# Performance work log

Hardware: AMD Instinct MI355X
Metric: run time of the kernel (lower is better)

Reference implementation:

```python
import jax, jax.numpy as jnp
import numpy as np

N_OBJECTS = 64
EMB = 64
N_PRED = 32
N_LAYERS = 3
BATCH = 128

# Ordered pairs (i, j), i != j, in the exact nested-loop order of the torch module
_pairs = np.array([(i, j) for i in range(N_OBJECTS) for j in range(N_OBJECTS) if i != j], dtype=np.int32)
IDX_I = jnp.asarray(_pairs[:, 0])  # [N*(N-1)]
IDX_J = jnp.asarray(_pairs[:, 1])


def setup_inputs() -> dict:
    key = jax.random.key(0)
    ks = jax.random.split(key, 5)
    return {
        "object_ids": jax.random.randint(ks[0], (BATCH, N_OBJECTS), 0, N_OBJECTS),
        "emb_table": jax.random.normal(ks[1], (N_OBJECTS, EMB), dtype=jnp.float32),
        "W1": jax.random.normal(ks[2], (N_LAYERS, EMB, 3 * EMB), dtype=jnp.float32) * 0.07,
        "b1": jnp.zeros((N_LAYERS, EMB), dtype=jnp.float32),
        "W2": jax.random.normal(ks[3], (N_LAYERS, N_PRED, EMB), dtype=jnp.float32) * 0.12,
        "b2": jnp.zeros((N_LAYERS, N_PRED), dtype=jnp.float32),
    }


def reference(object_ids, emb_table, W1, b1, W2, b2):
    e = emb_table[object_ids]                # [B, N, D] embedding lookup
    mean = e.mean(axis=1)                    # [B, D] — identical for every pair (torch recomputes it)
    B, _, D = e.shape
    P = IDX_I.shape[0]                       # N*(N-1) ordered pairs
    # triple = cat([e_i, e_j, mean]) for all ordered pairs, built once: [B, P, 3D]
    triple = jnp.concatenate(
        [e[:, IDX_I, :], e[:, IDX_J, :], jnp.broadcast_to(mean[:, None, :], (B, P, D))],
        axis=-1,
    )
    # All layers share the same triple input; batch all pairs into single GEMMs per layer.
    h = jax.nn.relu(jnp.einsum('bpc,ldc->lbpd', triple, W1) + b1[:, None, None, :])   # [L,B,P,D]
    preds = jax.nn.sigmoid(jnp.einsum('lbpd,lqd->lbpq', h, W2) + b2[:, None, None, :])  # [L,B,P,Q]
    return preds, e
```

## Files before the change

kernel.cpp:

```cpp
#include <hip/hip_runtime.h>
#include <hip/hip_bf16.h>
#include <math.h>

#define NL 3
#define NB 128
#define NO 64
#define ND 64
#define NQ 32
#define NP 4032

typedef __bf16 bf16x8 __attribute__((ext_vector_type(8)));
typedef float  f32x4  __attribute__((ext_vector_type(4)));

__device__ __forceinline__ float sigm(float x) {
  return __builtin_amdgcn_rcpf(1.0f + __expf(-x));
}

__global__ __launch_bounds__(256) void precomp_k(
    const int* __restrict__ ids, const float* __restrict__ emb,
    const float* __restrict__ W1, const float* __restrict__ b1,
    float* __restrict__ Ut, float* __restrict__ Vt, float* __restrict__ M,
    float* __restrict__ e_out)
{
  const int blk = blockIdx.x, tid = threadIdx.x;

  if (blk < NB) {
    __shared__ int   ids_s[NO];
    __shared__ float psum[4][ND];
    __shared__ float mean_s[ND];
    const int b = blk;
    if (tid < NO) ids_s[tid] = ids[b * NO + tid];
    __syncthreads();

    {
      const int d = tid & 63, ng = tid >> 6;
      float s = 0.f;
#pragma unroll
      for (int nn = 0; nn < 16; ++nn) {
        const int n = ng * 16 + nn;
        const float v = emb[ids_s[n] * ND + d];
        e_out[(b * NO + n) * ND + d] = v;
        s += v;
      }
      psum[ng][d] = s;
    }
    __syncthreads();
    if (tid < ND)
      mean_s[tid] = (psum[0][tid] + psum[1][tid] + psum[2][tid] + psum[3][tid]) * (1.0f / 64.0f);
    __syncthreads();

    if (tid < 192) {
      const int l = tid >> 6, d = tid & 63;
      const float* wrow = W1 + (l * ND + d) * 192 + 128;
      float acc = 0.f;
#pragma unroll
      for (int c4 = 0; c4 < 16; ++c4) {
        const f32x4 w = *(const f32x4*)(wrow + c4 * 4);
        const f32x4 m = *(const f32x4*)(&mean_s[c4 * 4]);
        acc += w[0] * m[0] + w[1] * m[1] + w[2] * m[2] + w[3] * m[3];
      }
      M[(l * NB + b) * ND + d] = acc + b1[l * ND + d];
    }
  } else {
    const int idx = blk - NB;
    const int l = idx >> 1, half = idx & 1;
    __shared__ float e_s[NO][68];
    {
      const int o = tid >> 2, c0 = (tid & 3) * 16;
      const float* er = emb + o * ND + c0;
#pragma unroll
      for (int c = 0; c < 16; c += 4)
        *(f32x4*)(&e_s[o][c0 + c]) = *(const f32x4*)(er + c);
    }
    __syncthreads();

    const int d = tid & 63, og = tid >> 6;
    const float* wrow = W1 + (l * ND + d) * 192 + half * 64;
    float acc[16];
#pragma unroll
    for (int k = 0; k < 16; ++k) acc[k] = 0.f;
#pragma unroll
    for (int c4 = 0; c4 < 16; ++c4) {
      const f32x4 w = *(const f32x4*)(wrow + c4 * 4);
#pragma unroll
      for (int oo = 0; oo < 16; ++oo) {
        const f32x4 e = *(const f32x4*)(&e_s[og * 16 + oo][c4 * 4]);
        acc[oo] += e[0] * w[0] + e[1] * w[1] + e[2] * w[2] + e[3] * w[3];
      }
    }
    float* T = half ? Vt : Ut;
#pragma unroll
    for (int oo = 0; oo < 16; ++oo)
      T[(l * NO + og * 16 + oo) * ND + d] = acc[oo];
  }
}

__global__ __launch_bounds__(256) void main_k(
    const int* __restrict__ ids, const float* __restrict__ W2,
    const float* __restrict__ b2,
    const float* __restrict__ Ut, const float* __restrict__ Vt,
    const float* __restrict__ M, float* __restrict__ out)
{
  __shared__ float UpM_s[NO * 68];
  __shared__ __align__(16) __bf16 Vb_s[NO * 64];

  const int blk = blockIdx.x, tid = threadIdx.x;
  const int ic = blk & 1, b = (blk >> 1) & 127, l = blk >> 8;

  {
    const int j = tid >> 2, kq = (tid & 3) * 16;
    const int oid = ids[b * NO + j];
    const float* vrow = Vt + (l * NO + oid) * ND + kq;
    const float* urow = Ut + (l * NO + oid) * ND + kq;
    const float* mrow = M + (l * NB + b) * ND + kq;
    f32x4 vv[4];
#pragma unroll
    for (int c = 0; c < 4; ++c) {
      vv[c] = *(const f32x4*)(vrow + c * 4);
      const f32x4 u = *(const f32x4*)(urow + c * 4);
      const f32x4 m = *(const f32x4*)(mrow + c * 4);
      *(f32x4*)(&UpM_s[j * 68 + kq + c * 4]) = u + m;
    }
    const int swz = (j & 7) << 4;
#pragma unroll
    for (int c = 0; c < 2; ++c) {
      bf16x8 pk;
#pragma unroll
      for (int e = 0; e < 4; ++e) pk[e] = (__bf16)vv[2 * c][e];
#pragma unroll
      for (int e = 0; e < 4; ++e) pk[4 + e] = (__bf16)vv[2 * c + 1][e];
      const int byteoff = j * 128 + (((kq + c * 8) * 2) ^ swz);
      *(bf16x8*)((char*)Vb_s + byteoff) = pk;
    }
  }

  const int lane = tid & 63;
  const int qlo = lane & 15, g = lane >> 4;
  bf16x8 bfrag[2][2];
  float b2v[2];
#pragma unroll
  for (int qt = 0; qt < 2; ++qt) {
    b2v[qt] = b2[l * NQ + qt * 16 + qlo];
#pragma unroll
    for (int kt = 0; kt < 2; ++kt) {
      const float* w2p = W2 + (l * NQ + qt * 16 + qlo) * ND + kt * 32 + g * 8;
      const f32x4 w0 = *(const f32x4*)(w2p);
      const f32x4 w1v = *(const f32x4*)(w2p + 4);
      bf16x8 bf;
#pragma unroll
      for (int e = 0; e < 4; ++e) bf[e] = (__bf16)w0[e];
#pragma unroll
      for (int e = 0; e < 4; ++e) bf[4 + e] = (__bf16)w1v[e];
      bfrag[qt][kt] = bf;
    }
  }
  __syncthreads();

  const int wave = tid >> 6;
  const int j0 = wave * 16;
  const int jA = j0 + qlo;
  const int swzA = (jA & 7) << 4;
  const char* vbase = (const char*)Vb_s + jA * 128;
  const int i0 = ic * 32;

  for (int ii = 0; ii < 32; ++ii) {
    const int i = i0 + ii;
    const float* upm = &UpM_s[i * 68];

    bf16x8 a[2];
#pragma unroll
    for (int kt = 0; kt < 2; ++kt) {
      const int k0 = g * 8 + kt * 32;
      const bf16x8 v8 = *(const bf16x8*)(vbase + ((k0 * 2) ^ swzA));
      const f32x4 r0 = *(const f32x4*)(upm + k0);
      const f32x4 r1 = *(const f32x4*)(upm + k0 + 4);
      bf16x8 t;
      t[0] = (__bf16)fmaxf((float)v8[0] + r0[0], 0.0f);
      t[1] = (__bf16)fmaxf((float)v8[1] + r0[1], 0.0f);
      t[2] = (__bf16)fmaxf((float)v8[2] + r0[2], 0.0f);
      t[3] = (__bf16)fmaxf((float)v8[3] + r0[3], 0.0f);
      t[4] = (__bf16)fmaxf((float)v8[4] + r1[0], 0.0f);
      t[5] = (__bf16)fmaxf((float)v8[5] + r1[1], 0.0f);
      t[6] = (__bf16)fmaxf((float)v8[6] + r1[2], 0.0f);
      t[7] = (__bf16)fmaxf((float)v8[7] + r1[3], 0.0f);
      a[kt] = t;
    }

    const f32x4 z = {0.f, 0.f, 0.f, 0.f};
    f32x4 acc0 = __builtin_amdgcn_mfma_f32_16x16x32_bf16(a[0], bfrag[0][0], z, 0, 0, 0);
    acc0 = __builtin_amdgcn_mfma_f32_16x16x32_bf16(a[1], bfrag[0][1], acc0, 0, 0, 0);
    f32x4 acc1 = __builtin_amdgcn_mfma_f32_16x16x32_bf16(a[0], bfrag[1][0], z, 0, 0, 0);
    acc1 = __builtin_amdgcn_mfma_f32_16x16x32_bf16(a[1], bfrag[1][1], acc1, 0, 0, 0);

    float* pb = out + ((size_t)(l * NB + b) * NP + (size_t)i * 63) * NQ;
#pragma unroll
    for (int r = 0; r < 4; ++r) {
      const int jrow = j0 + g * 4 + r;
      if (jrow != i) {
        const int p_in_i = (jrow < i) ? jrow : jrow - 1;
        float* o0 = pb + p_in_i * NQ + qlo;
        o0[0]  = sigm(acc0[r] + b2v[0]);
        o0[16] = sigm(acc1[r] + b2v[1]);
      }
    }
  }
}

extern "C" void kernel_launch(void* const* d_in, const int* in_sizes, int n_in,
                              void* d_out, int out_size, void* d_ws, size_t ws_size,
                              hipStream_t stream) {
  const int*   ids = (const int*)d_in[0];
  const float* emb = (const float*)d_in[1];
  const float* W1  = (const float*)d_in[2];
  const float* b1  = (const float*)d_in[3];
  const float* W2  = (const float*)d_in[4];
  const float* b2  = (const float*)d_in[5];
  float* out = (float*)d_out;

  float* Ut = (float*)d_ws;
  float* Vt = Ut + NL * NO * ND;
  float* M  = Vt + NL * NO * ND;
  float* e_out = out + (size_t)NL * NB * NP * NQ;

  precomp_k<<<NB + 2 * NL, 256, 0, stream>>>(ids, emb, W1, b1, Ut, Vt, M, e_out);
  main_k<<<NL * NB * 2, 256, 0, stream>>>(ids, W2, b2, Ut, Vt, M, out);
}
```

Measured before the change: 48.73 us.

## Fuse precompute into main kernel with per-block MFMA projections and vector stores

Merges the two kernels into one. Each block now recomputes the mean, the M projection and its own U/V embedding projections with bf16 MFMA instead of reading them from a workspace. The second GEMM is transposed so each lane holds four contiguous q outputs, which lets it write them as nontemporal 16-byte stores. This removes a kernel launch and the workspace round trip, at the cost of redundant per-block projection work and bf16 rounding of the first-layer projections.

```diff
diff --git a/kernel.cpp b/kernel.cpp
--- a/kernel.cpp
+++ b/kernel.cpp
@@ -1,6 +1,5 @@
 #include <hip/hip_runtime.h>
 #include <hip/hip_bf16.h>
-#include <math.h>
 
 #define NL 3
 #define NB 128
@@ -16,192 +15,145 @@
   return __builtin_amdgcn_rcpf(1.0f + __expf(-x));
 }
 
-__global__ __launch_bounds__(256) void precomp_k(
+__device__ __forceinline__ bf16x8 pack_bf16(const f32x4 a, const f32x4 b) {
+  bf16x8 r;
+  r[0] = (__bf16)a[0]; r[1] = (__bf16)a[1]; r[2] = (__bf16)a[2]; r[3] = (__bf16)a[3];
+  r[4] = (__bf16)b[0]; r[5] = (__bf16)b[1]; r[6] = (__bf16)b[2]; r[7] = (__bf16)b[3];
+  return r;
+}
+
+__global__ __launch_bounds__(256) void fused_k(
     const int* __restrict__ ids, const float* __restrict__ emb,
     const float* __restrict__ W1, const float* __restrict__ b1,
-    float* __restrict__ Ut, float* __restrict__ Vt, float* __restrict__ M,
-    float* __restrict__ e_out)
+    const float* __restrict__ W2, const float* __restrict__ b2,
+    float* __restrict__ out, float* __restrict__ e_out)
 {
-  const int blk = blockIdx.x, tid = threadIdx.x;
+  __shared__ int   ids_s[NO];
+  __shared__ float psum[4][ND];
+  __shared__ float mean_s[ND];
+  __shared__ float M_s[ND];
+  __shared__ float UpM_s[32 * 68];
+  __shared__ float V_s[NO * 68];
 
-  if (blk < NB) {
-    __shared__ int   ids_s[NO];
-    __shared__ float psum[4][ND];
-    __shared__ float mean_s[ND];
-    const int b = blk;
-    if (tid < NO) ids_s[tid] = ids[b * NO + tid];
-    __syncthreads();
+  const int tid = threadIdx.x, blk = blockIdx.x;
+  const int ic = blk & 1, b = (blk >> 1) & 127, l = blk >> 8;
+  const int lane = tid & 63, wave = tid >> 6;
+  const int qlo = lane & 15, g = lane >> 4;
 
-    {
-      const int d = tid & 63, ng = tid >> 6;
-      float s = 0.f;
-#pragma unroll
-      for (int nn = 0; nn < 16; ++nn) {
-        const int n = ng * 16 + nn;
-        const float v = emb[ids_s[n] * ND + d];
-        e_out[(b * NO + n) * ND + d] = v;
-        s += v;
-      }
-      psum[ng][d] = s;
-    }
-    __syncthreads();
-    if (tid < ND)
-      mean_s[tid] = (psum[0][tid] + psum[1][tid] + psum[2][tid] + psum[3][tid]) * (1.0f / 64.0f);
-    __syncthreads();
-
-    if (tid < 192) {
-      const int l = tid >> 6, d = tid & 63;
-      const float* wrow = W1 + (l * ND + d) * 192 + 128;
-      float acc = 0.f;
-#pragma unroll
-      for (int c4 = 0; c4 < 16; ++c4) {
-        const f32x4 w = *(const f32x4*)(wrow + c4 * 4);
-        const f32x4 m = *(const f32x4*)(&mean_s[c4 * 4]);
-        acc += w[0] * m[0] + w[1] * m[1] + w[2] * m[2] + w[3] * m[3];
-      }
-      M[(l * NB + b) * ND + d] = acc + b1[l * ND + d];
-    }
-  } else {
-    const int idx = blk - NB;
-    const int l = idx >> 1, half = idx & 1;
-    __shared__ float e_s[NO][68];
-    {
-      const int o = tid >> 2, c0 = (tid & 3) * 16;
-      const float* er = emb + o * ND + c0;
-#pragma unroll
-      for (int c = 0; c < 16; c += 4)
-        *(f32x4*)(&e_s[o][c0 + c]) = *(const f32x4*)(er + c);
-    }
-    __syncthreads();
-
-    const int d = tid & 63, og = tid >> 6;
-    const float* wrow = W1 + (l * ND + d) * 192 + half * 64;
-    float acc[16];
-#pragma unroll
-    for (int k = 0; k < 16; ++k) acc[k] = 0.f;
-#pragma unroll
-    for (int c4 = 0; c4 < 16; ++c4) {
-      const f32x4 w = *(const f32x4*)(wrow + c4 * 4);
-#pragma unroll
-      for (int oo = 0; oo < 16; ++oo) {
-        const f32x4 e = *(const f32x4*)(&e_s[og * 16 + oo][c4 * 4]);
-        acc[oo] += e[0] * w[0] + e[1] * w[1] + e[2] * w[2] + e[3] * w[3];
-      }
-    }
-    float* T = half ? Vt : Ut;
-#pragma unroll
-    for (int oo = 0; oo < 16; ++oo)
-      T[(l * NO + og * 16 + oo) * ND + d] = acc[oo];
-  }
-}
-
-__global__ __launch_bounds__(256) void main_k(
-    const int* __restrict__ ids, const float* __restrict__ W2,
-    const float* __restrict__ b2,
-    const float* __restrict__ Ut, const float* __restrict__ Vt,
-    const float* __restrict__ M, float* __restrict__ out)
-{
-  __shared__ float UpM_s[NO * 68];
-  __shared__ __align__(16) __bf16 Vb_s[NO * 64];
-
-  const int blk = blockIdx.x, tid = threadIdx.x;
-  const int ic = blk & 1, b = (blk >> 1) & 127, l = blk >> 8;
+  if (tid < NO) ids_s[tid] = ids[b * NO + tid];
+  __syncthreads();
 
   {
-    const int j = tid >> 2, kq = (tid & 3) * 16;
-    const int oid = ids[b * NO + j];
-    const float* vrow = Vt + (l * NO + oid) * ND + kq;
-    const float* urow = Ut + (l * NO + oid) * ND + kq;
-    const float* mrow = M + (l * NB + b) * ND + kq;
-    f32x4 vv[4];
+    const int d = lane;
+    float s = 0.f;
 #pragma unroll
-    for (int c = 0; c < 4; ++c) {
-      vv[c] = *(const f32x4*)(vrow + c * 4);
-      const f32x4 u = *(const f32x4*)(urow + c * 4);
-      const f32x4 m = *(const f32x4*)(mrow + c * 4);
-      *(f32x4*)(&UpM_s[j * 68 + kq + c * 4]) = u + m;
+    for (int nn = 0; nn < 16; ++nn) {
+      const int n = wave * 16 + nn;
+      const float v = emb[ids_s[n] * ND + d];
+      if (l == 0 && (n >> 5) == ic) e_out[(b * NO + n) * ND + d] = v;
+      s += v;
     }
-    const int swz = (j & 7) << 4;
+    psum[wave][d] = s;
+  }
+  __syncthreads();
+  if (tid < ND)
+    mean_s[tid] = (psum[0][tid] + psum[1][tid] + psum[2][tid] + psum[3][tid]) * (1.0f / 64.0f);
+  __syncthreads();
+
+  if (tid < ND) {
+    const float* wrow = W1 + (l * ND + tid) * 192 + 128;
+    float acc = 0.f;
 #pragma unroll
-    for (int c = 0; c < 2; ++c) {
-      bf16x8 pk;
-#pragma unroll
-      for (int e = 0; e < 4; ++e) pk[e] = (__bf16)vv[2 * c][e];
-#pragma unroll
-      for (int e = 0; e < 4; ++e) pk[4 + e] = (__bf16)vv[2 * c + 1][e];
-      const int byteoff = j * 128 + (((kq + c * 8) * 2) ^ swz);
-      *(bf16x8*)((char*)Vb_s + byteoff) = pk;
+    for (int c = 0; c < 16; ++c) {
+      const f32x4 w = *(const f32x4*)(wrow + c * 4);
+      const f32x4 m = *(const f32x4*)(&mean_s[c * 4]);
+      acc += w[0] * m[0] + w[1] * m[1] + w[2] * m[2] + w[3] * m[3];
     }
-  }
-
-  const int lane = tid & 63;
-  const int qlo = lane & 15, g = lane >> 4;
-  bf16x8 bfrag[2][2];
-  float b2v[2];
-#pragma unroll
-  for (int qt = 0; qt < 2; ++qt) {
-    b2v[qt] = b2[l * NQ + qt * 16 + qlo];
-#pragma unroll
-    for (int kt = 0; kt < 2; ++kt) {
-      const float* w2p = W2 + (l * NQ + qt * 16 + qlo) * ND + kt * 32 + g * 8;
-      const f32x4 w0 = *(const f32x4*)(w2p);
-      const f32x4 w1v = *(const f32x4*)(w2p + 4);
-      bf16x8 bf;
-#pragma unroll
-      for (int e = 0; e < 4; ++e) bf[e] = (__bf16)w0[e];
-#pragma unroll
-      for (int e = 0; e < 4; ++e) bf[4 + e] = (__bf16)w1v[e];
-      bfrag[qt][kt] = bf;
-    }
+    M_s[tid] = acc + b1[l * ND + tid];
   }
   __syncthreads();
 
-  const int wave = tid >> 6;
-  const int j0 = wave * 16;
-  const int jA = j0 + qlo;
-  const int swzA = (jA & 7) << 4;
-  const char* vbase = (const char*)Vb_s + jA * 128;
+#pragma unroll
+  for (int t6 = 0; t6 < 6; ++t6) {
+    const int t = wave * 6 + t6;
+    const bool isU = (t < 8);
+    const int rt = isU ? (2 * ic + (t >> 2)) : ((t - 8) >> 2);
+    const int dt = t & 3;
+    const int dcol = dt * 16 + qlo;
+    const float* arow = emb + ids_s[rt * 16 + qlo] * ND;
+    const float* brow = W1 + (l * ND + dcol) * 192 + (isU ? 0 : 64);
+    const float minit = isU ? M_s[dcol] : 0.f;
+    f32x4 acc = {minit, minit, minit, minit};
+#pragma unroll
+    for (int kh = 0; kh < 2; ++kh) {
+      const int k0 = kh * 32 + g * 8;
+      const bf16x8 af = pack_bf16(*(const f32x4*)(arow + k0), *(const f32x4*)(arow + k0 + 4));
+      const bf16x8 bf = pack_bf16(*(const f32x4*)(brow + k0), *(const f32x4*)(brow + k0 + 4));
+      acc = __builtin_amdgcn_mfma_f32_16x16x32_bf16(af, bf, acc, 0, 0, 0);
+    }
+    float* dst = isU ? &UpM_s[((t >> 2) * 16) * 68] : &V_s[(rt * 16) * 68];
+#pragma unroll
+    for (int r = 0; r < 4; ++r)
+      dst[(4 * g + r) * 68 + dcol] = acc[r];
+  }
+  __syncthreads();
+
+  const int jA = wave * 16 + qlo;
+  f32x4 vf[2][2];
+#pragma unroll
+  for (int kt = 0; kt < 2; ++kt) {
+    vf[kt][0] = *(const f32x4*)(&V_s[jA * 68 + kt * 32 + g * 8]);
+    vf[kt][1] = *(const f32x4*)(&V_s[jA * 68 + kt * 32 + g * 8 + 4]);
+  }
+  bf16x8 wfrag[2][2];
+#pragma unroll
+  for (int qt = 0; qt < 2; ++qt)
+#pragma unroll
+    for (int kt = 0; kt < 2; ++kt) {
+      const float* wp = W2 + (l * NQ + qt * 16 + qlo) * ND + kt * 32 + g * 8;
+      wfrag[qt][kt] = pack_bf16(*(const f32x4*)wp, *(const f32x4*)(wp + 4));
+    }
+  const f32x4 b20 = *(const f32x4*)(b2 + l * NQ + g * 4);
+  const f32x4 b21 = *(const f32x4*)(b2 + l * NQ + 16 + g * 4);
+
   const int i0 = ic * 32;
+  float* outb = out + (size_t)(l * NB + b) * NP * NQ;
 
   for (int ii = 0; ii < 32; ++ii) {
-    const int i = i0 + ii;
-    const float* upm = &UpM_s[i * 68];
-
-    bf16x8 a[2];
+    const float* upm = &UpM_s[ii * 68];
+    bf16x8 hb[2];
 #pragma unroll
     for (int kt = 0; kt < 2; ++kt) {
-      const int k0 = g * 8 + kt * 32;
-      const bf16x8 v8 = *(const bf16x8*)(vbase + ((k0 * 2) ^ swzA));
+      const int k0 = kt * 32 + g * 8;
       const f32x4 r0 = *(const f32x4*)(upm + k0);
       const f32x4 r1 = *(const f32x4*)(upm + k0 + 4);
-      bf16x8 t;
-      t[0] = (__bf16)fmaxf((float)v8[0] + r0[0], 0.0f);
-      t[1] = (__bf16)fmaxf((float)v8[1] + r0[1], 0.0f);
-      t[2] = (__bf16)fmaxf((float)v8[2] + r0[2], 0.0f);
-      t[3] = (__bf16)fmaxf((float)v8[3] + r0[3], 0.0f);
-      t[4] = (__bf16)fmaxf((float)v8[4] + r1[0], 0.0f);
-      t[5] = (__bf16)fmaxf((float)v8[5] + r1[1], 0.0f);
-      t[6] = (__bf16)fmaxf((float)v8[6] + r1[2], 0.0f);
-      t[7] = (__bf16)fmaxf((float)v8[7] + r1[3], 0.0f);
-      a[kt] = t;
+      f32x4 h0, h1;
+#pragma unroll
+      for (int e = 0; e < 4; ++e) {
+        h0[e] = fmaxf(vf[kt][0][e] + r0[e], 0.0f);
+        h1[e] = fmaxf(vf[kt][1][e] + r1[e], 0.0f);
+      }
+      hb[kt] = pack_bf16(h0, h1);
     }
 
     const f32x4 z = {0.f, 0.f, 0.f, 0.f};
-    f32x4 acc0 = __builtin_amdgcn_mfma_f32_16x16x32_bf16(a[0], bfrag[0][0], z, 0, 0, 0);
-    acc0 = __builtin_amdgcn_mfma_f32_16x16x32_bf16(a[1], bfrag[0][1], acc0, 0, 0, 0);
-    f32x4 acc1 = __builtin_amdgcn_mfma_f32_16x16x32_bf16(a[0], bfrag[1][0], z, 0, 0, 0);
-    acc1 = __builtin_amdgcn_mfma_f32_16x16x32_bf16(a[1], bfrag[1][1], acc1, 0, 0, 0);
+    f32x4 acc0 = __builtin_amdgcn_mfma_f32_16x16x32_bf16(wfrag[0][0], hb[0], z, 0, 0, 0);
+    acc0 = __builtin_amdgcn_mfma_f32_16x16x32_bf16(wfrag[0][1], hb[1], acc0, 0, 0, 0);
+    f32x4 acc1 = __builtin_amdgcn_mfma_f32_16x16x32_bf16(wfrag[1][0], hb[0], z, 0, 0, 0);
+    acc1 = __builtin_amdgcn_mfma_f32_16x16x32_bf16(wfrag[1][1], hb[1], acc1, 0, 0, 0);
 
-    float* pb = out + ((size_t)(l * NB + b) * NP + (size_t)i * 63) * NQ;
+    const int i = i0 + ii;
+    if (jA != i) {
+      const int p = (jA < i) ? jA : jA - 1;
+      float* base = outb + ((size_t)i * 63 + p) * NQ + g * 4;
+      f32x4 o0, o1;
 #pragma unroll
-    for (int r = 0; r < 4; ++r) {
-      const int jrow = j0 + g * 4 + r;
-      if (jrow != i) {
-        const int p_in_i = (jrow < i) ? jrow : jrow - 1;
-        float* o0 = pb + p_in_i * NQ + qlo;
-        o0[0]  = sigm(acc0[r] + b2v[0]);
-        o0[16] = sigm(acc1[r] + b2v[1]);
+      for (int r = 0; r < 4; ++r) {
+        o0[r] = sigm(acc0[r] + b20[r]);
+        o1[r] = sigm(acc1[r] + b21[r]);
       }
+      __builtin_nontemporal_store(o0, (f32x4*)base);
+      __builtin_nontemporal_store(o1, (f32x4*)(base + 16));
     }
   }
 }
@@ -216,12 +168,7 @@
   const float* W2  = (const float*)d_in[4];
   const float* b2  = (const float*)d_in[5];
   float* out = (float*)d_out;
-
-  float* Ut = (float*)d_ws;
-  float* Vt = Ut + NL * NO * ND;
-  float* M  = Vt + NL * NO * ND;
   float* e_out = out + (size_t)NL * NB * NP * NQ;
 
-  precomp_k<<<NB + 2 * NL, 256, 0, stream>>>(ids, emb, W1, b1, Ut, Vt, M, e_out);
-  main_k<<<NL * NB * 2, 256, 0, stream>>>(ids, W2, b2, Ut, Vt, M, out);
+  fused_k<<<NL * NB * 2, 256, 0, stream>>>(ids, emb, W1, b1, W2, b2, out, e_out);
 }
```

Result: slower. 81.24 us (+66.7%).
